# Kernel optimization log

Measured on AMD Instinct MI355X. Metric: run time of the kernel, lower is better.

Reference implementation:

```python
import jax, jax.numpy as jnp
import numpy as np

B, S, D, H = 4, 1024, 512, 8
EPS = 1e-5


def _cx(x):
    # [..., 2] float -> complex
    return jax.lax.complex(x[..., 0], x[..., 1])


def setup_inputs() -> dict:
    key = jax.random.key(0)
    ks = jax.random.split(key, 9)
    f = lambda k, sh: jax.random.normal(k, sh, dtype=jnp.float32)
    inp = {
        "q": f(ks[0], (B, S, D, 2)),
        "k": f(ks[1], (B, S, D, 2)),
        "v": f(ks[2], (B, S, D, 2)),
        "Wq": f(ks[3], (D, D, 2)) * 0.02,
        "bq": f(ks[4], (D, 2)) * 0.02,
        "Wk": f(ks[5], (D, D, 2)) * 0.02,
        "bk": f(ks[6], (D, 2)) * 0.02,
        "Wv": f(ks[7], (D, D, 2)) * 0.02,
        "bv": f(ks[8], (D, 2)) * 0.02,
        "gamma_r": jnp.ones((D,), jnp.float32),
        "beta_r": jnp.zeros((D,), jnp.float32),
        "gamma_i": jnp.ones((D,), jnp.float32),
        "beta_i": jnp.zeros((D,), jnp.float32),
        "n_heads": H,
    }
    return inp


def _layernorm(x, g, b):
    # torch LayerNorm: biased variance, eps inside sqrt
    mu = jnp.mean(x, axis=-1, keepdims=True)
    var = jnp.mean((x - mu) ** 2, axis=-1, keepdims=True)
    return (x - mu) / jnp.sqrt(var + EPS) * g + b


def reference(q, k, v, Wq, bq, Wk, bk, Wv, bv, gamma_r, beta_r, gamma_i, beta_i, n_heads):
    qc, kc, vc = _cx(q), _cx(k), _cx(v)
    # complex linear: x @ W^T + b
    Q = jnp.einsum("bsd,ed->bse", qc, _cx(Wq)) + _cx(bq)
    K = jnp.einsum("bsd,ed->bse", kc, _cx(Wk)) + _cx(bk)
    V = jnp.einsum("bsd,ed->bse", vc, _cx(Wv)) + _cx(bv)
    b, s, d = qc.shape
    dh = d // n_heads
    Qh = Q.reshape(b, s, n_heads, dh)
    Kh = K.reshape(b, s, n_heads, dh)
    Vh = V.reshape(b, s, n_heads, dh)
    # complex scores [b,h,q,k], scaled by sqrt(dh)
    scores = jnp.einsum("bqhd,bkhd->bhqk", Qh, Kh) / jnp.sqrt(jnp.float32(dh))
    # original: softmax over view_as_real dim=-2 == key axis, real & imag independently
    attn = jax.lax.complex(jax.nn.softmax(scores.real, axis=-1),
                           jax.nn.softmax(scores.imag, axis=-1))
    # (dropout is identity in eval mode)
    out = jnp.einsum("bhqk,bkhd->bqhd", attn, Vh).reshape(b, s, d)
    out = out + qc  # residual
    out_r = _layernorm(out.real, gamma_r, beta_r)
    out_i = _layernorm(out.imag, gamma_i, beta_i)
    return jnp.stack([out_r, out_i], axis=-1)  # [B,S,D,2]
```

## Files before the change

### kernel.cpp

```cpp
#include <hip/hip_runtime.h>
#include <math.h>

#define BB  4
#define SS  1024
#define DD  512
#define HH  8
#define DHD 64
#define PL  2097152
#define WPL 262144

constexpr float LN_EPS = 1e-5f;

using half4 = __attribute__((ext_vector_type(4))) _Float16;
using half8 = __attribute__((ext_vector_type(8))) _Float16;
using f32x4 = __attribute__((ext_vector_type(4))) float;

__device__ __forceinline__ half8 negh(half8 a) {
    union { half8 h; unsigned int u[4]; } t;
    t.h = a;
    #pragma unroll
    for (int i = 0; i < 4; ++i) t.u[i] ^= 0x80008000u;
    return t.h;
}
__device__ __forceinline__ half8 ldh64(const unsigned short* p, int row, int col) {
    return *(const half8*)(p + row * 64 + (col ^ ((row & 7) << 3)));
}
__device__ __forceinline__ unsigned int cvtpk(float a, float b) {
    union { decltype(__builtin_amdgcn_cvt_pkrtz(0.f, 0.f)) v; unsigned int u; } t;
    t.v = __builtin_amdgcn_cvt_pkrtz(a, b);
    return t.u;
}
__device__ __forceinline__ float ex2(float x) { return __builtin_amdgcn_exp2f(x); }
#define MFMA16(acc, a, b) acc = __builtin_amdgcn_mfma_f32_16x16x32_f16(a, b, acc, 0, 0, 0)

__global__ __launch_bounds__(256)
void cvt_kernel(const float2* __restrict__ s0, const float2* __restrict__ s1,
                const float2* __restrict__ s2, unsigned short* __restrict__ dst,
                int planeElems) {
    const int z = blockIdx.y;
    const float2* src = z == 0 ? s0 : (z == 1 ? s1 : s2);
    unsigned short* base = dst + (size_t)z * 2 * planeElems;
    const int idx = (blockIdx.x * 256 + threadIdx.x) * 2;
    float4 t = *(const float4*)(src + idx);
    const int m = idx >> 9;
    const int d = idx & 511;
    const int ob = (((m >> 7) << 3) + (d >> 6)) * 8192 + ((m & 127) << 6) + (d & 63);
    union { _Float16 h[2]; unsigned int u; } r, i;
    r.h[0] = (_Float16)t.x; r.h[1] = (_Float16)t.z;
    i.h[0] = (_Float16)t.y; i.h[1] = (_Float16)t.w;
    *(unsigned int*)(base + ob) = r.u;
    *(unsigned int*)(base + planeElems + ob) = i.u;
}

__global__ __launch_bounds__(256, 3)
void proj_kernel(const unsigned short* __restrict__ XP,
                 const unsigned short* __restrict__ WP,
                 const float2* __restrict__ bq, const float2* __restrict__ bk,
                 const float2* __restrict__ bv,
                 unsigned short* __restrict__ QG, unsigned short* __restrict__ KG,
                 unsigned short* __restrict__ VG) {
    const unsigned short* XR = XP + (size_t)blockIdx.z * 2 * PL;
    const unsigned short* XI = XR + PL;
    const unsigned short* WRp = WP + (size_t)blockIdx.z * 2 * WPL;
    const unsigned short* WIp = WRp + WPL;
    const float2* bias; unsigned short* outP;
    if (blockIdx.z == 0)      { bias = bq; outP = QG; }
    else if (blockIdx.z == 1) { bias = bk; outP = KG; }
    else                      { bias = bv; outP = VG; }
    const bool isV = (blockIdx.z == 2);

    __shared__ __align__(16) unsigned short Xs[2][64 * 64];
    __shared__ __align__(16) unsigned short Ws[2][128 * 64];

    const int tid  = threadIdx.x;
    const int w    = tid >> 6;
    const int lane = tid & 63;
    const int quad = lane >> 4;
    const int l15  = lane & 15;
    const int wm   = w >> 1;
    const int we   = w & 1;
    const int m0   = blockIdx.x * 64;
    const int e0   = blockIdx.y * 128;

    const int srow8 = lane >> 3;
    const int sg    = lane & 7;
    const int swz   = ((sg ^ srow8) << 3);
    const int xbase = ((m0 >> 7) << 16) + ((m0 & 127) << 6);
    const int wbase = ((e0 >> 7) << 16);
    const unsigned short* gsX  = XR  + xbase + srow8 * 64 + swz;
    const unsigned short* gsW0 = WRp + wbase + srow8 * 64 + swz;
    const unsigned short* gsW1 = WIp + wbase + srow8 * 64 + swz;

#define GLD(SRC, DST) __builtin_amdgcn_global_load_lds( \
        (const __attribute__((address_space(1))) void*)(SRC), \
        (__attribute__((address_space(3))) void*)(DST), 16, 0, 0)

    f32x4 Sr[2][4], Si[2][4];
    #pragma unroll
    for (int a = 0; a < 2; ++a)
        #pragma unroll
        for (int c = 0; c < 4; ++c) { Sr[a][c] = (f32x4)0.f; Si[a][c] = (f32x4)0.f; }

    for (int s = 0; s < 8; ++s) {
        if (s) __syncthreads();
        if (w == 0) {
            const unsigned short* g = gsX + s * 8192;
            #pragma unroll
            for (int jj = 0; jj < 16; ++jj)
                GLD(g + (jj >> 3) * PL + (jj & 7) * 512, &Xs[jj >> 3][(jj & 7) * 512]);
        } else if (w == 1) {
            const unsigned short* g = gsW0 + s * 8192;
            #pragma unroll
            for (int jj = 0; jj < 16; ++jj)
                GLD(g + jj * 512, &Ws[0][jj * 512]);
        } else if (w == 2) {
            const unsigned short* g = gsW1 + s * 8192;
            #pragma unroll
            for (int jj = 0; jj < 16; ++jj)
                GLD(g + jj * 512, &Ws[1][jj * 512]);
        }
        __syncthreads();

        #pragma unroll
        for (int kc = 0; kc < 2; ++kc) {
            const int dl = kc * 32 + quad * 8;
            half8 xr[2], xi[2];
            #pragma unroll
            for (int mf = 0; mf < 2; ++mf) {
                const int mr = wm * 32 + mf * 16 + l15;
                xr[mf] = ldh64(Xs[0], mr, dl);
                xi[mf] = ldh64(Xs[1], mr, dl);
            }
            #pragma unroll
            for (int ef = 0; ef < 4; ++ef) {
                const int er = we * 64 + ef * 16 + l15;
                half8 wr  = ldh64(Ws[0], er, dl);
                half8 wi  = ldh64(Ws[1], er, dl);
                half8 wmi = negh(wi);
                #pragma unroll
                for (int mf = 0; mf < 2; ++mf) {
                    MFMA16(Sr[mf][ef], xr[mf], wr);
                    MFMA16(Sr[mf][ef], xi[mf], wmi);
                    MFMA16(Si[mf][ef], xr[mf], wi);
                    MFMA16(Si[mf][ef], xi[mf], wr);
                }
            }
        }
    }
#undef GLD

    #pragma unroll
    for (int ef = 0; ef < 4; ++ef) {
        const int eg  = e0 + we * 64 + ef * 16 + l15;
        const int hh  = eg >> 6;
        const int col = eg & 63;
        float2 bb = bias[eg];
        #pragma unroll
        for (int mf = 0; mf < 2; ++mf) {
            #pragma unroll
            for (int reg = 0; reg < 4; ++reg) {
                int m = m0 + wm * 32 + mf * 16 + quad * 4 + reg;
                int bidx = m >> 10;
                int sidx = m & 1023;
                int bh = bidx * HH + hh;
                union { _Float16 h; unsigned short u; } cr, ci;
                cr.h = (_Float16)(Sr[mf][ef][reg] + bb.x);
                ci.h = (_Float16)(Si[mf][ef][reg] + bb.y);
                size_t o = isV ? ((size_t)bh * DHD + col) * SS + sidx
                               : ((size_t)bh * SS + sidx) * DHD + col;
                outP[0 * PL + o] = cr.u;
                outP[1 * PL + o] = ci.u;
            }
        }
    }
}

#define AWID 72
__global__ __launch_bounds__(256, 2)
void attn_kernel(const unsigned short* __restrict__ QG, const unsigned short* __restrict__ KG,
                 const unsigned short* __restrict__ VG,
                 unsigned short* __restrict__ ObR, unsigned short* __restrict__ ObI) {
    __shared__ __align__(16) unsigned short Ks[2][2][64 * 64];
    __shared__ __align__(16) unsigned short Vt[2][64 * 64];
    __shared__ __align__(16) unsigned short Ps[2][64 * AWID];
    __shared__ float lbuf[2][2][64];

    const int n   = blockIdx.x;
    const int bh  = (n & 7) * 4 + (n >> 7);
    const int q0  = ((n >> 3) & 15) * 64;
    const int b   = bh >> 3;
    const int h   = bh & 7;

    const int tid  = threadIdx.x;
    const int w    = tid >> 6;
    const int lane = tid & 63;
    const int quad = lane >> 4;
    const int l15  = lane & 15;
    const int sw   = w & 1;
    const int tw   = w >> 1;

    const int srow = lane >> 3;
    const int sg   = lane & 7;
    const bool isK = (w < 2);
    const unsigned short* bpK = nullptr;
    const unsigned short* bpV = nullptr;
    unsigned short* ldV = nullptr;
    if (isK) {
        bpK = KG + (size_t)w * PL + (size_t)bh * SS * DHD + srow * DHD + ((sg ^ srow) << 3);
    } else {
        bpV = VG + (size_t)(w - 2) * PL + (size_t)bh * DHD * SS + srow * SS + ((sg ^ srow) << 3);
        ldV = &Vt[w - 2][0];
    }

#define GLD(SRC, DST) __builtin_amdgcn_global_load_lds( \
        (const __attribute__((address_space(1))) void*)(SRC), \
        (__attribute__((address_space(3))) void*)(DST), 16, 0, 0)

    if (isK) {
        unsigned short* ld = &Ks[0][w][0];
        #pragma unroll
        for (int j = 0; j < 8; ++j) GLD(bpK + j * 8 * DHD, ld + j * 512);
    }

    half8 qfr[2][2], qfi[2][2], qfmi[2][2];
    #pragma unroll
    for (int qt = 0; qt < 2; ++qt)
        #pragma unroll
        for (int kc = 0; kc < 2; ++kc) {
            size_t qa = ((size_t)bh * SS + q0 + sw * 32 + qt * 16 + l15) * DHD + kc * 32 + quad * 8;
            qfr[qt][kc]  = *(const half8*)(QG + qa);
            qfi[qt][kc]  = *(const half8*)(QG + PL + qa);
            qfmi[qt][kc] = negh(qfi[qt][kc]);
        }

    f32x4 acc[2][2][4];
    #pragma unroll
    for (int qt = 0; qt < 2; ++qt)
        #pragma unroll
        for (int dt = 0; dt < 2; ++dt)
            #pragma unroll
            for (int p = 0; p < 4; ++p) acc[qt][dt][p] = (f32x4)0.f;
    float lacc[2][2] = {{0.f, 0.f}, {0.f, 0.f}};

    constexpr float EC = 0.18033688011112042f;

    __syncthreads();

    const unsigned short* Kr_c = &Ks[0][0][0];
    const unsigned short* Ki_c = &Ks[0][1][0];
    const unsigned short* Kr_n = &Ks[1][0][0];
    const unsigned short* Ki_n = &Ks[1][1][0];
    unsigned short* kst_nxt = isK ? &Ks[1][w][0] : nullptr;
    unsigned short* kst_alt = isK ? &Ks[0][w][0] : nullptr;

    for (int t = 0; t < 16; ++t) {
        if (isK) {
            if (t < 15) {
                const unsigned short* g = bpK + (size_t)(t + 1) * 64 * DHD;
                #pragma unroll
                for (int j = 0; j < 8; ++j) GLD(g + j * 8 * DHD, kst_nxt + j * 512);
            }
        } else {
            const unsigned short* g = bpV + (size_t)t * 64;
            #pragma unroll
            for (int j = 0; j < 8; ++j) GLD(g + j * 8 * SS, ldV + j * 512);
        }

        f32x4 Sr[2][2], Si[2][2];
        #pragma unroll
        for (int a = 0; a < 2; ++a)
            #pragma unroll
            for (int c = 0; c < 2; ++c) { Sr[a][c] = (f32x4)0.f; Si[a][c] = (f32x4)0.f; }
        #pragma unroll
        for (int kc = 0; kc < 2; ++kc) {
            const int dl = kc * 32 + quad * 8;
            #pragma unroll
            for (int kt2 = 0; kt2 < 2; ++kt2) {
                const int krow = tw * 32 + kt2 * 16 + l15;
                half8 akr = ldh64(Kr_c, krow, dl);
                half8 aki = ldh64(Ki_c, krow, dl);
                #pragma unroll
                for (int qt = 0; qt < 2; ++qt) {
                    MFMA16(Sr[kt2][qt], akr, qfr[qt][kc]);
                    MFMA16(Sr[kt2][qt], aki, qfmi[qt][kc]);
                    MFMA16(Si[kt2][qt], aki, qfr[qt][kc]);
                    MFMA16(Si[kt2][qt], akr, qfi[qt][kc]);
                }
            }
        }

        #pragma unroll
        for (int kt2 = 0; kt2 < 2; ++kt2)
            #pragma unroll
            for (int qt = 0; qt < 2; ++qt) {
                float er0 = ex2(Sr[kt2][qt][0] * EC), er1 = ex2(Sr[kt2][qt][1] * EC);
                float er2 = ex2(Sr[kt2][qt][2] * EC), er3 = ex2(Sr[kt2][qt][3] * EC);
                float ei0 = ex2(Si[kt2][qt][0] * EC), ei1 = ex2(Si[kt2][qt][1] * EC);
                float ei2 = ex2(Si[kt2][qt][2] * EC), ei3 = ex2(Si[kt2][qt][3] * EC);
                lacc[qt][0] += (er0 + er1) + (er2 + er3);
                lacc[qt][1] += (ei0 + ei1) + (ei2 + ei3);
                const int qrow = sw * 32 + qt * 16 + l15;
                const int kcol = tw * 32 + kt2 * 16 + quad * 4;
                uint2 pr, pi;
                pr.x = cvtpk(er0, er1); pr.y = cvtpk(er2, er3);
                pi.x = cvtpk(ei0, ei1); pi.y = cvtpk(ei2, ei3);
                *(uint2*)&Ps[0][qrow * AWID + kcol] = pr;
                *(uint2*)&Ps[1][qrow * AWID + kcol] = pi;
            }

        asm volatile("s_waitcnt lgkmcnt(0)" ::: "memory");
        if (!isK) asm volatile("s_waitcnt vmcnt(0)" ::: "memory");
        __builtin_amdgcn_s_barrier();
        asm volatile("" ::: "memory");

        #pragma unroll
        for (int kc = 0; kc < 2; ++kc) {
            half8 ap[2][2];
            #pragma unroll
            for (int qt = 0; qt < 2; ++qt) {
                const int qrow = sw * 32 + qt * 16 + l15;
                ap[qt][0] = *(const half8*)&Ps[0][qrow * AWID + kc * 32 + quad * 8];
                ap[qt][1] = *(const half8*)&Ps[1][qrow * AWID + kc * 32 + quad * 8];
            }
            #pragma unroll
            for (int dt = 0; dt < 2; ++dt) {
                const int drow = tw * 32 + dt * 16 + l15;
                half8 bvr = ldh64(Vt[0], drow, kc * 32 + quad * 8);
                half8 bvi = ldh64(Vt[1], drow, kc * 32 + quad * 8);
                #pragma unroll
                for (int qt = 0; qt < 2; ++qt) {
                    MFMA16(acc[qt][dt][0], ap[qt][0], bvr);
                    MFMA16(acc[qt][dt][1], ap[qt][0], bvi);
                    MFMA16(acc[qt][dt][2], ap[qt][1], bvr);
                    MFMA16(acc[qt][dt][3], ap[qt][1], bvi);
                }
            }
        }

        if (isK) asm volatile("s_waitcnt vmcnt(0)" ::: "memory");
        __builtin_amdgcn_s_barrier();
        asm volatile("" ::: "memory");

        const unsigned short* tr;
        tr = Kr_c; Kr_c = Kr_n; Kr_n = tr;
        tr = Ki_c; Ki_c = Ki_n; Ki_n = tr;
        unsigned short* ts = kst_nxt; kst_nxt = kst_alt; kst_alt = ts;
    }
#undef GLD

    #pragma unroll
    for (int qt = 0; qt < 2; ++qt)
        #pragma unroll
        for (int p = 0; p < 2; ++p) {
            float v = lacc[qt][p];
            v += __shfl_xor(v, 16);
            v += __shfl_xor(v, 32);
            if (lane < 16) lbuf[p][tw][sw * 32 + qt * 16 + lane] = v;
        }
    __syncthreads();

    #pragma unroll
    for (int qt = 0; qt < 2; ++qt)
        #pragma unroll
        for (int reg = 0; reg < 4; ++reg) {
            const int qloc = sw * 32 + qt * 16 + quad * 4 + reg;
            const float ir = 1.f / (lbuf[0][0][qloc] + lbuf[0][1][qloc]);
            const float ii = 1.f / (lbuf[1][0][qloc] + lbuf[1][1][qloc]);
            #pragma unroll
            for (int dt = 0; dt < 2; ++dt) {
                const int d = tw * 32 + dt * 16 + l15;
                union { _Float16 h; unsigned short u; } cr, ci;
                cr.h = (_Float16)(acc[qt][dt][0][reg] * ir - acc[qt][dt][3][reg] * ii);
                ci.h = (_Float16)(acc[qt][dt][1][reg] * ir + acc[qt][dt][2][reg] * ii);
                size_t o = ((size_t)b * SS + q0 + qloc) * DD + h * DHD + d;
                ObR[o] = cr.u;
                ObI[o] = ci.u;
            }
        }
}

__global__ __launch_bounds__(256)
void ln_kernel(const unsigned short* __restrict__ OrP, const unsigned short* __restrict__ OiP,
               const float2* __restrict__ Qin,
               const float* __restrict__ gr, const float* __restrict__ br,
               const float* __restrict__ gi, const float* __restrict__ bi,
               float2* __restrict__ out) {
    const int row = blockIdx.x;
    const int tid = threadIdx.x;
    const size_t base = (size_t)row * DD;
    const int e0 = 2 * tid, e1 = 2 * tid + 1;

    union { unsigned int u; _Float16 h[2]; } tr, ti;
    tr.u = *(const unsigned int*)(OrP + base + e0);
    ti.u = *(const unsigned int*)(OiP + base + e0);
    float2 r0 = Qin[base + e0];
    float2 r1 = Qin[base + e1];
    float xr0 = (float)tr.h[0] + r0.x;
    float xr1 = (float)tr.h[1] + r1.x;
    float xi0 = (float)ti.h[0] + r0.y;
    float xi1 = (float)ti.h[1] + r1.y;

    float sr = xr0 + xr1;
    float si = xi0 + xi1;
    float qr = xr0 * xr0 + xr1 * xr1;
    float qi = xi0 * xi0 + xi1 * xi1;
    #pragma unroll
    for (int off = 32; off > 0; off >>= 1) {
        sr += __shfl_down(sr, off);
        si += __shfl_down(si, off);
        qr += __shfl_down(qr, off);
        qi += __shfl_down(qi, off);
    }
    __shared__ float red[4][4];
    __shared__ float stat[4];
    int lane = tid & 63, wid = tid >> 6;
    if (lane == 0) { red[wid][0] = sr; red[wid][1] = si; red[wid][2] = qr; red[wid][3] = qi; }
    __syncthreads();
    if (tid == 0) {
        sr = red[0][0] + red[1][0] + red[2][0] + red[3][0];
        si = red[0][1] + red[1][1] + red[2][1] + red[3][1];
        qr = red[0][2] + red[1][2] + red[2][2] + red[3][2];
        qi = red[0][3] + red[1][3] + red[2][3] + red[3][3];
        float mur = sr * (1.f / DD), mui = si * (1.f / DD);
        float vr = qr * (1.f / DD) - mur * mur;
        float vi = qi * (1.f / DD) - mui * mui;
        stat[0] = mur; stat[1] = mui;
        stat[2] = rsqrtf(vr + LN_EPS); stat[3] = rsqrtf(vi + LN_EPS);
    }
    __syncthreads();
    float mur = stat[0], mui = stat[1], rsr = stat[2], rsi = stat[3];
    out[base + e0] = make_float2((xr0 - mur) * rsr * gr[e0] + br[e0],
                                 (xi0 - mui) * rsi * gi[e0] + bi[e0]);
    out[base + e1] = make_float2((xr1 - mur) * rsr * gr[e1] + br[e1],
                                 (xi1 - mui) * rsi * gi[e1] + bi[e1]);
}

extern "C" void kernel_launch(void* const* d_in, const int* in_sizes, int n_in,
                              void* d_out, int out_size, void* d_ws, size_t ws_size,
                              hipStream_t stream) {
    const float2* q  = (const float2*)d_in[0];
    const float2* k  = (const float2*)d_in[1];
    const float2* v  = (const float2*)d_in[2];
    const float2* Wq = (const float2*)d_in[3];
    const float2* bq = (const float2*)d_in[4];
    const float2* Wk = (const float2*)d_in[5];
    const float2* bk = (const float2*)d_in[6];
    const float2* Wv = (const float2*)d_in[7];
    const float2* bv = (const float2*)d_in[8];
    const float*  gr = (const float*)d_in[9];
    const float*  br = (const float*)d_in[10];
    const float*  gi = (const float*)d_in[11];
    const float*  bi = (const float*)d_in[12];

    unsigned short* XP  = (unsigned short*)d_ws;
    unsigned short* WP  = XP + (size_t)6 * PL;
    unsigned short* QG  = WP + (size_t)6 * WPL;
    unsigned short* KG  = QG + (size_t)2 * PL;
    unsigned short* VG  = KG + (size_t)2 * PL;
    unsigned short* ObR = VG + (size_t)2 * PL;
    unsigned short* ObI = ObR + (size_t)PL;

    cvt_kernel<<<dim3(4096, 3), 256, 0, stream>>>(q, k, v, XP, PL);
    cvt_kernel<<<dim3(512, 3), 256, 0, stream>>>(Wq, Wk, Wv, WP, WPL);
    proj_kernel<<<dim3(64, 4, 3), 256, 0, stream>>>(XP, WP, bq, bk, bv, QG, KG, VG);
    attn_kernel<<<dim3(512), 256, 0, stream>>>(QG, KG, VG, ObR, ObI);
    ln_kernel<<<dim3(BB * SS), 256, 0, stream>>>(ObR, ObI, q, gr, br, gi, bi, (float2*)d_out);
}
```

Before: 205.9 us.

## Give each wave 16 full query rows and keep P in registers via bpermute

The attention kernel is reorganized so each of the four waves owns 16 query rows across all 64 keys and all 64 head dims, instead of a 2x2 split over query and key/dim halves. The exponentiated scores stay in registers and are rearranged into MFMA operand layout with ds_bpermute, which removes the shared-memory P buffer, its LDS round trip and one barrier per tile. V is now double-buffered alongside K, and the softmax scale is folded into Q in fp16 up front. In exchange, K and V fragments are reloaded per wave with no sharing across waves, accumulator register pressure rises, and pre-scaling Q in fp16 loses some precision.

```diff
diff --git a/kernel.cpp b/kernel.cpp
--- a/kernel.cpp
+++ b/kernel.cpp
@@ -175,15 +175,13 @@
     }
 }
 
-#define AWID 72
 __global__ __launch_bounds__(256, 2)
 void attn_kernel(const unsigned short* __restrict__ QG, const unsigned short* __restrict__ KG,
                  const unsigned short* __restrict__ VG,
                  unsigned short* __restrict__ ObR, unsigned short* __restrict__ ObI) {
     __shared__ __align__(16) unsigned short Ks[2][2][64 * 64];
-    __shared__ __align__(16) unsigned short Vt[2][64 * 64];
-    __shared__ __align__(16) unsigned short Ps[2][64 * AWID];
-    __shared__ float lbuf[2][2][64];
+    __shared__ __align__(16) unsigned short Vt[2][2][64 * 64];
+    __shared__ float lbuf[2][4][16];
 
     const int n   = blockIdx.x;
     const int bh  = (n & 7) * 4 + (n >> 7);
@@ -196,187 +194,155 @@
     const int lane = tid & 63;
     const int quad = lane >> 4;
     const int l15  = lane & 15;
-    const int sw   = w & 1;
-    const int tw   = w >> 1;
 
     const int srow = lane >> 3;
     const int sg   = lane & 7;
     const bool isK = (w < 2);
-    const unsigned short* bpK = nullptr;
-    const unsigned short* bpV = nullptr;
-    unsigned short* ldV = nullptr;
+    const unsigned short* bp;
+    unsigned short *ld0, *ld1;
+    int jstr, ktmul;
     if (isK) {
-        bpK = KG + (size_t)w * PL + (size_t)bh * SS * DHD + srow * DHD + ((sg ^ srow) << 3);
+        bp = KG + (size_t)w * PL + (size_t)bh * SS * DHD + srow * DHD + ((sg ^ srow) << 3);
+        jstr = 8 * DHD; ktmul = DHD;
+        ld0 = &Ks[0][w][0]; ld1 = &Ks[1][w][0];
     } else {
-        bpV = VG + (size_t)(w - 2) * PL + (size_t)bh * DHD * SS + srow * SS + ((sg ^ srow) << 3);
-        ldV = &Vt[w - 2][0];
+        bp = VG + (size_t)(w - 2) * PL + (size_t)bh * DHD * SS + srow * SS + ((sg ^ srow) << 3);
+        jstr = 8 * SS; ktmul = 1;
+        ld0 = &Vt[0][w - 2][0]; ld1 = &Vt[1][w - 2][0];
     }
 
 #define GLD(SRC, DST) __builtin_amdgcn_global_load_lds( \
         (const __attribute__((address_space(1))) void*)(SRC), \
         (__attribute__((address_space(3))) void*)(DST), 16, 0, 0)
 
-    if (isK) {
-        unsigned short* ld = &Ks[0][w][0];
-        #pragma unroll
-        for (int j = 0; j < 8; ++j) GLD(bpK + j * 8 * DHD, ld + j * 512);
-    }
-
-    half8 qfr[2][2], qfi[2][2], qfmi[2][2];
-    #pragma unroll
-    for (int qt = 0; qt < 2; ++qt)
-        #pragma unroll
-        for (int kc = 0; kc < 2; ++kc) {
-            size_t qa = ((size_t)bh * SS + q0 + sw * 32 + qt * 16 + l15) * DHD + kc * 32 + quad * 8;
-            qfr[qt][kc]  = *(const half8*)(QG + qa);
-            qfi[qt][kc]  = *(const half8*)(QG + PL + qa);
-            qfmi[qt][kc] = negh(qfi[qt][kc]);
-        }
-
-    f32x4 acc[2][2][4];
-    #pragma unroll
-    for (int qt = 0; qt < 2; ++qt)
-        #pragma unroll
-        for (int dt = 0; dt < 2; ++dt)
-            #pragma unroll
-            for (int p = 0; p < 4; ++p) acc[qt][dt][p] = (f32x4)0.f;
-    float lacc[2][2] = {{0.f, 0.f}, {0.f, 0.f}};
+    #pragma unroll
+    for (int j = 0; j < 8; ++j) GLD(bp + j * jstr, ld0 + j * 512);
 
     constexpr float EC = 0.18033688011112042f;
+    half8 qfr[2], qfi[2], qfmi[2];
+    #pragma unroll
+    for (int kc = 0; kc < 2; ++kc) {
+        size_t qa = ((size_t)bh * SS + q0 + w * 16 + l15) * DHD + kc * 32 + quad * 8;
+        half8 r = *(const half8*)(QG + qa);
+        half8 i = *(const half8*)(QG + PL + qa);
+        const _Float16 ech = (_Float16)EC;
+        #pragma unroll
+        for (int e = 0; e < 8; ++e) { r[e] *= ech; i[e] *= ech; }
+        qfr[kc] = r; qfi[kc] = i; qfmi[kc] = negh(i);
+    }
+
+    f32x4 acc[4][4];
+    #pragma unroll
+    for (int dt = 0; dt < 4; ++dt)
+        #pragma unroll
+        for (int p = 0; p < 4; ++p) acc[dt][p] = (f32x4)0.f;
+    float lacc[2] = {0.f, 0.f};
+
+    const int idx_lo = (l15 + ((quad & 1) << 5)) << 2;
+    const int idx_hi = idx_lo + 64;
 
     __syncthreads();
 
-    const unsigned short* Kr_c = &Ks[0][0][0];
-    const unsigned short* Ki_c = &Ks[0][1][0];
-    const unsigned short* Kr_n = &Ks[1][0][0];
-    const unsigned short* Ki_n = &Ks[1][1][0];
-    unsigned short* kst_nxt = isK ? &Ks[1][w][0] : nullptr;
-    unsigned short* kst_alt = isK ? &Ks[0][w][0] : nullptr;
-
     for (int t = 0; t < 16; ++t) {
-        if (isK) {
-            if (t < 15) {
-                const unsigned short* g = bpK + (size_t)(t + 1) * 64 * DHD;
-                #pragma unroll
-                for (int j = 0; j < 8; ++j) GLD(g + j * 8 * DHD, kst_nxt + j * 512);
-            }
-        } else {
-            const unsigned short* g = bpV + (size_t)t * 64;
-            #pragma unroll
-            for (int j = 0; j < 8; ++j) GLD(g + j * 8 * SS, ldV + j * 512);
-        }
-
-        f32x4 Sr[2][2], Si[2][2];
-        #pragma unroll
-        for (int a = 0; a < 2; ++a)
-            #pragma unroll
-            for (int c = 0; c < 2; ++c) { Sr[a][c] = (f32x4)0.f; Si[a][c] = (f32x4)0.f; }
+        const int cur = t & 1;
+        if (t < 15) {
+            const unsigned short* g = bp + (size_t)(t + 1) * 64 * ktmul;
+            unsigned short* ld = cur ? ld0 : ld1;
+            #pragma unroll
+            for (int j = 0; j < 8; ++j) GLD(g + j * jstr, ld + j * 512);
+        }
+        const unsigned short* Krc = &Ks[cur][0][0];
+        const unsigned short* Kic = &Ks[cur][1][0];
+        const unsigned short* Vrc = &Vt[cur][0][0];
+        const unsigned short* Vic = &Vt[cur][1][0];
+
+        f32x4 Sr[4], Si[4];
+        #pragma unroll
+        for (int kt = 0; kt < 4; ++kt) { Sr[kt] = (f32x4)0.f; Si[kt] = (f32x4)0.f; }
         #pragma unroll
         for (int kc = 0; kc < 2; ++kc) {
             const int dl = kc * 32 + quad * 8;
             #pragma unroll
-            for (int kt2 = 0; kt2 < 2; ++kt2) {
-                const int krow = tw * 32 + kt2 * 16 + l15;
-                half8 akr = ldh64(Kr_c, krow, dl);
-                half8 aki = ldh64(Ki_c, krow, dl);
-                #pragma unroll
-                for (int qt = 0; qt < 2; ++qt) {
-                    MFMA16(Sr[kt2][qt], akr, qfr[qt][kc]);
-                    MFMA16(Sr[kt2][qt], aki, qfmi[qt][kc]);
-                    MFMA16(Si[kt2][qt], aki, qfr[qt][kc]);
-                    MFMA16(Si[kt2][qt], akr, qfi[qt][kc]);
-                }
-            }
-        }
-
-        #pragma unroll
-        for (int kt2 = 0; kt2 < 2; ++kt2)
-            #pragma unroll
-            for (int qt = 0; qt < 2; ++qt) {
-                float er0 = ex2(Sr[kt2][qt][0] * EC), er1 = ex2(Sr[kt2][qt][1] * EC);
-                float er2 = ex2(Sr[kt2][qt][2] * EC), er3 = ex2(Sr[kt2][qt][3] * EC);
-                float ei0 = ex2(Si[kt2][qt][0] * EC), ei1 = ex2(Si[kt2][qt][1] * EC);
-                float ei2 = ex2(Si[kt2][qt][2] * EC), ei3 = ex2(Si[kt2][qt][3] * EC);
-                lacc[qt][0] += (er0 + er1) + (er2 + er3);
-                lacc[qt][1] += (ei0 + ei1) + (ei2 + ei3);
-                const int qrow = sw * 32 + qt * 16 + l15;
-                const int kcol = tw * 32 + kt2 * 16 + quad * 4;
-                uint2 pr, pi;
-                pr.x = cvtpk(er0, er1); pr.y = cvtpk(er2, er3);
-                pi.x = cvtpk(ei0, ei1); pi.y = cvtpk(ei2, ei3);
-                *(uint2*)&Ps[0][qrow * AWID + kcol] = pr;
-                *(uint2*)&Ps[1][qrow * AWID + kcol] = pi;
-            }
-
-        asm volatile("s_waitcnt lgkmcnt(0)" ::: "memory");
-        if (!isK) asm volatile("s_waitcnt vmcnt(0)" ::: "memory");
+            for (int kt = 0; kt < 4; ++kt) {
+                half8 akr = ldh64(Krc, kt * 16 + l15, dl);
+                half8 aki = ldh64(Kic, kt * 16 + l15, dl);
+                MFMA16(Sr[kt], akr, qfr[kc]);
+                MFMA16(Sr[kt], aki, qfmi[kc]);
+                MFMA16(Si[kt], aki, qfr[kc]);
+                MFMA16(Si[kt], akr, qfi[kc]);
+            }
+        }
+
+        unsigned int ar[4][2], ai[4][2];
+        #pragma unroll
+        for (int kt = 0; kt < 4; ++kt) {
+            float er0 = ex2(Sr[kt][0]), er1 = ex2(Sr[kt][1]);
+            float er2 = ex2(Sr[kt][2]), er3 = ex2(Sr[kt][3]);
+            float ei0 = ex2(Si[kt][0]), ei1 = ex2(Si[kt][1]);
+            float ei2 = ex2(Si[kt][2]), ei3 = ex2(Si[kt][3]);
+            lacc[0] += (er0 + er1) + (er2 + er3);
+            lacc[1] += (ei0 + ei1) + (ei2 + ei3);
+            ar[kt][0] = cvtpk(er0, er1); ar[kt][1] = cvtpk(er2, er3);
+            ai[kt][0] = cvtpk(ei0, ei1); ai[kt][1] = cvtpk(ei2, ei3);
+        }
+
+        #pragma unroll
+        for (int kc = 0; kc < 2; ++kc) {
+            union { unsigned int u[4]; half8 h; } pr_, pi_;
+            #pragma unroll
+            for (int tt = 0; tt < 4; ++tt) {
+                const int idx = (tt >> 1) ? idx_hi : idx_lo;
+                const int hh  = tt & 1;
+                int rlo = __builtin_amdgcn_ds_bpermute(idx, (int)ar[2 * kc][hh]);
+                int rhi = __builtin_amdgcn_ds_bpermute(idx, (int)ar[2 * kc + 1][hh]);
+                int ilo = __builtin_amdgcn_ds_bpermute(idx, (int)ai[2 * kc][hh]);
+                int ihi = __builtin_amdgcn_ds_bpermute(idx, (int)ai[2 * kc + 1][hh]);
+                pr_.u[tt] = (quad >> 1) ? (unsigned int)rhi : (unsigned int)rlo;
+                pi_.u[tt] = (quad >> 1) ? (unsigned int)ihi : (unsigned int)ilo;
+            }
+            #pragma unroll
+            for (int dt = 0; dt < 4; ++dt) {
+                half8 bvr = ldh64(Vrc, dt * 16 + l15, kc * 32 + quad * 8);
+                half8 bvi = ldh64(Vic, dt * 16 + l15, kc * 32 + quad * 8);
+                MFMA16(acc[dt][0], pr_.h, bvr);
+                MFMA16(acc[dt][1], pr_.h, bvi);
+                MFMA16(acc[dt][2], pi_.h, bvr);
+                MFMA16(acc[dt][3], pi_.h, bvi);
+            }
+        }
+
+        asm volatile("s_waitcnt vmcnt(0)" ::: "memory");
         __builtin_amdgcn_s_barrier();
         asm volatile("" ::: "memory");
-
-        #pragma unroll
-        for (int kc = 0; kc < 2; ++kc) {
-            half8 ap[2][2];
-            #pragma unroll
-            for (int qt = 0; qt < 2; ++qt) {
-                const int qrow = sw * 32 + qt * 16 + l15;
-                ap[qt][0] = *(const half8*)&Ps[0][qrow * AWID + kc * 32 + quad * 8];
-                ap[qt][1] = *(const half8*)&Ps[1][qrow * AWID + kc * 32 + quad * 8];
-            }
-            #pragma unroll
-            for (int dt = 0; dt < 2; ++dt) {
-                const int drow = tw * 32 + dt * 16 + l15;
-                half8 bvr = ldh64(Vt[0], drow, kc * 32 + quad * 8);
-                half8 bvi = ldh64(Vt[1], drow, kc * 32 + quad * 8);
-                #pragma unroll
-                for (int qt = 0; qt < 2; ++qt) {
-                    MFMA16(acc[qt][dt][0], ap[qt][0], bvr);
-                    MFMA16(acc[qt][dt][1], ap[qt][0], bvi);
-                    MFMA16(acc[qt][dt][2], ap[qt][1], bvr);
-                    MFMA16(acc[qt][dt][3], ap[qt][1], bvi);
-                }
-            }
-        }
-
-        if (isK) asm volatile("s_waitcnt vmcnt(0)" ::: "memory");
-        __builtin_amdgcn_s_barrier();
-        asm volatile("" ::: "memory");
-
-        const unsigned short* tr;
-        tr = Kr_c; Kr_c = Kr_n; Kr_n = tr;
-        tr = Ki_c; Ki_c = Ki_n; Ki_n = tr;
-        unsigned short* ts = kst_nxt; kst_nxt = kst_alt; kst_alt = ts;
     }
 #undef GLD
 
     #pragma unroll
-    for (int qt = 0; qt < 2; ++qt)
-        #pragma unroll
-        for (int p = 0; p < 2; ++p) {
-            float v = lacc[qt][p];
-            v += __shfl_xor(v, 16);
-            v += __shfl_xor(v, 32);
-            if (lane < 16) lbuf[p][tw][sw * 32 + qt * 16 + lane] = v;
-        }
+    for (int p = 0; p < 2; ++p) {
+        float v = lacc[p];
+        v += __shfl_xor(v, 16);
+        v += __shfl_xor(v, 32);
+        if (lane < 16) lbuf[p][w][lane] = v;
+    }
     __syncthreads();
 
     #pragma unroll
-    for (int qt = 0; qt < 2; ++qt)
-        #pragma unroll
-        for (int reg = 0; reg < 4; ++reg) {
-            const int qloc = sw * 32 + qt * 16 + quad * 4 + reg;
-            const float ir = 1.f / (lbuf[0][0][qloc] + lbuf[0][1][qloc]);
-            const float ii = 1.f / (lbuf[1][0][qloc] + lbuf[1][1][qloc]);
-            #pragma unroll
-            for (int dt = 0; dt < 2; ++dt) {
-                const int d = tw * 32 + dt * 16 + l15;
-                union { _Float16 h; unsigned short u; } cr, ci;
-                cr.h = (_Float16)(acc[qt][dt][0][reg] * ir - acc[qt][dt][3][reg] * ii);
-                ci.h = (_Float16)(acc[qt][dt][1][reg] * ir + acc[qt][dt][2][reg] * ii);
-                size_t o = ((size_t)b * SS + q0 + qloc) * DD + h * DHD + d;
-                ObR[o] = cr.u;
-                ObI[o] = ci.u;
-            }
-        }
+    for (int reg = 0; reg < 4; ++reg) {
+        const int qq   = quad * 4 + reg;
+        const int qloc = w * 16 + qq;
+        const float ir = 1.f / lbuf[0][w][qq];
+        const float ii = 1.f / lbuf[1][w][qq];
+        #pragma unroll
+        for (int dt = 0; dt < 4; ++dt) {
+            const int d = dt * 16 + l15;
+            union { _Float16 h; unsigned short u; } cr, ci;
+            cr.h = (_Float16)(acc[dt][0][reg] * ir - acc[dt][3][reg] * ii);
+            ci.h = (_Float16)(acc[dt][1][reg] * ir + acc[dt][2][reg] * ii);
+            size_t o = ((size_t)b * SS + q0 + qloc) * DD + h * DHD + d;
+            ObR[o] = cr.u;
+            ObI[o] = ci.u;
+        }
+    }
 }
 
 __global__ __launch_bounds__(256)
```

Result: faster. 199.5 us (-3.1%).
